# Optimization experiments

Measured on AMD Instinct MI355X. Metric: run time of the kernel, lower is better.

The kernel has to match this reference:

```python
import jax, jax.numpy as jnp
import numpy as np

D = 512
H = 8
HD = D // H
EPS = 1e-8


def setup_inputs() -> dict:
    key = jax.random.key(0)
    ks = jax.random.split(key, 16)
    B, S = 4, 2048
    s = lambda n: 1.0 / np.sqrt(n)
    inp = {
        "gene_emb": jax.random.normal(ks[0], (B, S, D), jnp.float32),
        "expr_emb": jax.random.normal(ks[1], (B, S, D), jnp.float32),
        "M": jax.random.uniform(ks[2], (B, S, S), jnp.float32),
        # weights stored (in, out) so y = x @ W + b
        "W_fused": jax.random.normal(ks[3], (2 * D, D), jnp.float32) * s(2 * D),
        "b_fused": jnp.zeros((D,), jnp.float32),
        "W_Q": jax.random.normal(ks[4], (D, D), jnp.float32) * s(D),
        "b_Q": jnp.zeros((D,), jnp.float32),
        "W_K": jax.random.normal(ks[5], (D, D), jnp.float32) * s(D),
        "b_K": jnp.zeros((D,), jnp.float32),
        "W_V": jax.random.normal(ks[6], (D, D), jnp.float32) * s(D),
        "b_V": jnp.zeros((D,), jnp.float32),
        "W_O": jax.random.normal(ks[7], (D, D), jnp.float32) * s(D),
        "b_O": jnp.zeros((D,), jnp.float32),
    }
    return inp


def reference(gene_emb, expr_emb, M, W_fused, b_fused, W_Q, b_Q, W_K, b_K, W_V, b_V, W_O, b_O):
    B, S, _ = gene_emb.shape
    scale = HD ** (-0.5)
    fused = jnp.concatenate([gene_emb, expr_emb], axis=-1) @ W_fused + b_fused
    # (B,S,D) -> (B,H,S,HD)
    split = lambda x: x.reshape(B, S, H, HD).transpose(0, 2, 1, 3)
    Q = split(fused @ W_Q + b_Q)
    K = split(fused @ W_K + b_K)
    V = split(expr_emb @ W_V + b_V)
    scores = jnp.einsum("bhqd,bhkd->bhqk", Q, K) * scale
    Mg = M[:, None, :, :]  # broadcast over heads
    scores = scores * Mg
    attn = jax.nn.softmax(scores, axis=-1)
    A_sparse = attn * Mg
    norm = jnp.sum(jnp.abs(A_sparse), axis=-1, keepdims=True) + EPS
    A_bar = A_sparse / norm
    out = jnp.einsum("bhqk,bhkd->bhqd", A_bar, V)
    out = out.transpose(0, 2, 1, 3).reshape(B, S, D)
    return out @ W_O + b_O
```

## Files before the change

kernel.cpp:

```cpp
#include <hip/hip_runtime.h>

typedef unsigned short u16;
typedef __attribute__((ext_vector_type(8))) short bf16x8_t;
typedef __attribute__((ext_vector_type(4))) float f32x4_t;

__device__ __forceinline__ u16 f2bf(float x){
  union { float f; unsigned u; } v; v.f = x;
  unsigned r = v.u + 0x7FFFu + ((v.u >> 16) & 1u);
  return (u16)(r >> 16);
}
__device__ __forceinline__ float bf2f(u16 h){
  union { unsigned u; float f; } v; v.u = ((unsigned)h) << 16;
  return v.f;
}
__device__ __forceinline__ u16 hi16(float x){
  union { float f; unsigned u; } v; v.f = x;
  return (u16)(v.u >> 16);
}

__device__ __forceinline__ void gl2lds16(const u16* g, u16* l){
  __builtin_amdgcn_global_load_lds((const __attribute__((address_space(1))) void*)g,
                                   (__attribute__((address_space(3))) void*)l, 16, 0, 0);
}

__global__ __launch_bounds__(256) void prep_kernel(
    const float* __restrict__ gene, const float* __restrict__ expr,
    const float* __restrict__ Wf, const float* __restrict__ Wq,
    const float* __restrict__ Wk, const float* __restrict__ Wv,
    const float* __restrict__ Wo,
    u16* __restrict__ Xh, u16* __restrict__ Xl,
    u16* __restrict__ Wfth, u16* __restrict__ Wftl,
    u16* __restrict__ Wqth, u16* __restrict__ Wkth,
    u16* __restrict__ Wvth, u16* __restrict__ Woth)
{
  __shared__ float t[64][65];
  int tid = threadIdx.x;
  if (blockIdx.x < 8192){
    size_t e = ((size_t)blockIdx.x * 256 + tid) * 4;
    int row = (int)(e >> 10);
    int col = (int)(e & 1023);
    const float* src = (col < 512) ? (gene + (size_t)row * 512 + col)
                                   : (expr + (size_t)row * 512 + (col - 512));
    float4 v = *(const float4*)src;
    float a[4] = {v.x, v.y, v.z, v.w};
    u16 hs[4], ls[4];
#pragma unroll
    for (int i = 0; i < 4; i++){
      hs[i] = f2bf(a[i]);
      ls[i] = f2bf(a[i] - bf2f(hs[i]));
    }
    *(uint2*)(Xh + e) = make_uint2(hs[0] | ((unsigned)hs[1] << 16), hs[2] | ((unsigned)hs[3] << 16));
    *(uint2*)(Xl + e) = make_uint2(ls[0] | ((unsigned)ls[1] << 16), ls[2] | ((unsigned)ls[3] << 16));
    return;
  }
  int id = blockIdx.x - 8192;
  const float* W; u16* Th; u16* Tl; int K, kx, ny;
  if (id < 128){ W = Wf; Th = Wfth; Tl = Wftl; K = 1024; kx = id >> 3; ny = id & 7; }
  else {
    int tt = id - 128; int wi = tt >> 6; tt &= 63; kx = tt >> 3; ny = tt & 7; K = 512;
    W  = (wi == 0) ? Wq  : (wi == 1) ? Wk  : (wi == 2) ? Wv  : Wo;
    Th = (wi == 0) ? Wqth: (wi == 1) ? Wkth: (wi == 2) ? Wvth: Woth;
    Tl = nullptr;
  }
  int k0 = kx * 64, n0 = ny * 64;
  int r = tid >> 4;
  int c4 = (tid & 15) * 4;
#pragma unroll
  for (int p = 0; p < 4; p++){
    int k = p * 16 + r;
    float4 v = *(const float4*)(W + (size_t)(k0 + k) * 512 + n0 + c4);
    t[c4 + 0][k] = v.x; t[c4 + 1][k] = v.y; t[c4 + 2][k] = v.z; t[c4 + 3][k] = v.w;
  }
  __syncthreads();
#pragma unroll
  for (int p = 0; p < 4; p++){
    int n = p * 16 + r;
    u16 hs[4], ls[4];
#pragma unroll
    for (int i = 0; i < 4; i++){
      float x = t[n][c4 + i];
      hs[i] = f2bf(x);
      ls[i] = f2bf(x - bf2f(hs[i]));
    }
    size_t o = (size_t)(n0 + n) * K + k0 + c4;
    *(uint2*)(Th + o) = make_uint2(hs[0] | ((unsigned)hs[1] << 16), hs[2] | ((unsigned)hs[3] << 16));
    if (Tl)
      *(uint2*)(Tl + o) = make_uint2(ls[0] | ((unsigned)ls[1] << 16), ls[2] | ((unsigned)ls[3] << 16));
  }
}

template<int SPLITS>
__device__ __forceinline__ void gemm_core(
    const u16* __restrict__ Ah, const u16* __restrict__ Al, int lda,
    const u16* __restrict__ Bh, const u16* __restrict__ Bl, int K,
    int m0, int n0, f32x4_t (&acc)[4][2],
    u16* sAh, u16* sAl, u16* sBh, u16* sBl)
{
  int tid = threadIdx.x;
  int lane = tid & 63, w = tid >> 6, quad = lane >> 4, l15 = lane & 15;
  int wm = w & 1, wn = w >> 1;
  int lrow = lane >> 2;
  int swzS = ((lane >> 2) & 3) ^ ((lane >> 4) & 3);
  int gkq  = ((lane & 3) ^ swzS) * 8;
  const u16* pA0 = Ah + (size_t)(m0 + w * 32 + lrow) * lda + gkq;
  const u16* pA1 = Ah + (size_t)(m0 + w * 32 + 16 + lrow) * lda + gkq;
  const u16* pL0 = (SPLITS >= 2) ? Al + (size_t)(m0 + w * 32 + lrow) * lda + gkq : nullptr;
  const u16* pL1 = (SPLITS >= 2) ? Al + (size_t)(m0 + w * 32 + 16 + lrow) * lda + gkq : nullptr;
  const u16* pB0 = Bh + (size_t)(n0 + w * 16 + lrow) * K + gkq;
  const u16* pBl = (SPLITS == 3) ? Bl + (size_t)(n0 + w * 16 + lrow) * K + gkq : nullptr;
  u16* dA  = sAh + w * 1024;
  u16* dAl = (SPLITS >= 2) ? sAl + w * 1024 : nullptr;
  u16* dB  = sBh + w * 512;
  u16* dBl = (SPLITS == 3) ? sBl + w * 512 : nullptr;
  int pq = (quad ^ ((l15 & 3) ^ ((l15 >> 2) & 3))) * 8;

  for (int k0 = 0; k0 < K; k0 += 64){
    __syncthreads();
#pragma unroll
    for (int hf = 0; hf < 2; hf++){
      gl2lds16(pA0 + k0 + hf * 32, dA + hf * 4096);
      gl2lds16(pA1 + k0 + hf * 32, dA + hf * 4096 + 512);
      if constexpr (SPLITS >= 2){
        gl2lds16(pL0 + k0 + hf * 32, dAl + hf * 4096);
        gl2lds16(pL1 + k0 + hf * 32, dAl + hf * 4096 + 512);
      }
      gl2lds16(pB0 + k0 + hf * 32, dB + hf * 2048);
      if constexpr (SPLITS == 3)
        gl2lds16(pBl + k0 + hf * 32, dBl + hf * 2048);
    }
    __syncthreads();

#pragma unroll
    for (int hf = 0; hf < 2; hf++){
      bf16x8_t aH[4], aL[4], bH[2], bL[2];
#pragma unroll
      for (int mi = 0; mi < 4; mi++){
        int ad = (wm * 64 + mi * 16 + l15) * 32 + pq + hf * 4096;
        aH[mi] = *(const bf16x8_t*)&sAh[ad];
        if constexpr (SPLITS >= 2) aL[mi] = *(const bf16x8_t*)&sAl[ad];
      }
#pragma unroll
      for (int ni = 0; ni < 2; ni++){
        int bd = (wn * 32 + ni * 16 + l15) * 32 + pq + hf * 2048;
        bH[ni] = *(const bf16x8_t*)&sBh[bd];
        if constexpr (SPLITS == 3) bL[ni] = *(const bf16x8_t*)&sBl[bd];
      }
#pragma unroll
      for (int mi = 0; mi < 4; mi++)
#pragma unroll
        for (int ni = 0; ni < 2; ni++){
          acc[mi][ni] = __builtin_amdgcn_mfma_f32_16x16x32_bf16(aH[mi], bH[ni], acc[mi][ni], 0, 0, 0);
          if constexpr (SPLITS == 3)
            acc[mi][ni] = __builtin_amdgcn_mfma_f32_16x16x32_bf16(aH[mi], bL[ni], acc[mi][ni], 0, 0, 0);
          if constexpr (SPLITS >= 2)
            acc[mi][ni] = __builtin_amdgcn_mfma_f32_16x16x32_bf16(aL[mi], bH[ni], acc[mi][ni], 0, 0, 0);
        }
    }
  }
}

__global__ __launch_bounds__(256, 2) void gemm_fused_kernel(
    const u16* __restrict__ Xh, const u16* __restrict__ Xl,
    const u16* __restrict__ Wfth, const u16* __restrict__ Wftl,
    const float* __restrict__ bias, u16* __restrict__ Fh, u16* __restrict__ Fl)
{
  __shared__ __align__(16) u16 sAh[128 * 64], sAl[128 * 64], sBh[64 * 64], sBl[64 * 64];
  int m0 = blockIdx.x * 128, n0 = blockIdx.y * 64;
  f32x4_t acc[4][2];
#pragma unroll
  for (int i = 0; i < 4; i++)
#pragma unroll
    for (int j = 0; j < 2; j++)
#pragma unroll
      for (int r = 0; r < 4; r++) acc[i][j][r] = 0.f;
  gemm_core<3>(Xh, Xl, 1024, Wfth, Wftl, 1024, m0, n0, acc, sAh, sAl, sBh, sBl);

  int lane = threadIdx.x & 63, w = threadIdx.x >> 6, quad = lane >> 4, l15 = lane & 15;
  int wm = w & 1, wn = w >> 1;
#pragma unroll
  for (int mi = 0; mi < 4; mi++)
#pragma unroll
    for (int ni = 0; ni < 2; ni++){
      int gn = n0 + wn * 32 + ni * 16 + l15;
      float bs = bias[gn];
      int gm0 = m0 + wm * 64 + mi * 16 + quad * 4;
#pragma unroll
      for (int r = 0; r < 4; r++){
        float v = acc[mi][ni][r] + bs;
        u16 hb = f2bf(v);
        Fh[(size_t)(gm0 + r) * 512 + gn] = hb;
        Fl[(size_t)(gm0 + r) * 512 + gn] = f2bf(v - bf2f(hb));
      }
    }
}

__global__ __launch_bounds__(256, 2) void gemm_qkv_kernel(
    const u16* __restrict__ Fh, const u16* __restrict__ Fl,
    const u16* __restrict__ Xeh, const u16* __restrict__ Xel,
    const u16* __restrict__ Wqth, const u16* __restrict__ Wkth, const u16* __restrict__ Wvth,
    const float* __restrict__ bq, const float* __restrict__ bk, const float* __restrict__ bv,
    u16* __restrict__ Q, u16* __restrict__ Kout, u16* __restrict__ Vt, float qsc)
{
  __shared__ __align__(16) u16 sAh[128 * 64], sAl[128 * 64], sBh[64 * 64];
  int side = blockIdx.y >> 3;
  int m0 = blockIdx.x * 128, n0 = (blockIdx.y & 7) * 64;
  const u16* Ah = (side == 2) ? Xeh : Fh;
  const u16* Al = (side == 2) ? Xel : Fl;
  int lda = (side == 2) ? 1024 : 512;
  const u16* Bh = (side == 0) ? Wqth : (side == 1) ? Wkth : Wvth;
  const float* bias = (side == 0) ? bq : (side == 1) ? bk : bv;

  f32x4_t acc[4][2];
#pragma unroll
  for (int i = 0; i < 4; i++)
#pragma unroll
    for (int j = 0; j < 2; j++)
#pragma unroll
      for (int r = 0; r < 4; r++) acc[i][j][r] = 0.f;
  gemm_core<2>(Ah, Al, lda, Bh, nullptr, 512, m0, n0, acc, sAh, sAl, sBh, nullptr);

  int lane = threadIdx.x & 63, w = threadIdx.x >> 6, quad = lane >> 4, l15 = lane & 15;
  int wm = w & 1, wn = w >> 1;
#pragma unroll
  for (int mi = 0; mi < 4; mi++)
#pragma unroll
    for (int ni = 0; ni < 2; ni++){
      int gn = n0 + wn * 32 + ni * 16 + l15;
      float bs = bias[gn];
      int gm0 = m0 + wm * 64 + mi * 16 + quad * 4;
#pragma unroll
      for (int r = 0; r < 4; r++){
        float v = acc[mi][ni][r] + bs;
        int gm = gm0 + r;
        if (side == 0){
          Q[(size_t)gm * 512 + gn] = f2bf(v * qsc);
        } else if (side == 1){
          Kout[(size_t)gm * 512 + gn] = f2bf(v);
        } else {
          int bb = gm >> 11, s = gm & 2047;
          int hh = gn >> 6, d = gn & 63;
          Vt[((size_t)((bb * 8 + hh) * 64 + d) << 11) + s] = f2bf(v);
        }
      }
    }
}

__global__ __launch_bounds__(256, 2) void gemm_o_kernel(
    const u16* __restrict__ Oh, const u16* __restrict__ Woth,
    const float* __restrict__ bias, float* __restrict__ out)
{
  __shared__ __align__(16) u16 sAh[128 * 64], sBh[64 * 64];
  int m0 = blockIdx.x * 128, n0 = blockIdx.y * 64;
  f32x4_t acc[4][2];
#pragma unroll
  for (int i = 0; i < 4; i++)
#pragma unroll
    for (int j = 0; j < 2; j++)
#pragma unroll
      for (int r = 0; r < 4; r++) acc[i][j][r] = 0.f;
  gemm_core<1>(Oh, nullptr, 512, Woth, nullptr, 512, m0, n0, acc, sAh, nullptr, sBh, nullptr);

  int lane = threadIdx.x & 63, w = threadIdx.x >> 6, quad = lane >> 4, l15 = lane & 15;
  int wm = w & 1, wn = w >> 1;
#pragma unroll
  for (int mi = 0; mi < 4; mi++)
#pragma unroll
    for (int ni = 0; ni < 2; ni++){
      int gn = n0 + wn * 32 + ni * 16 + l15;
      float bs = bias[gn];
      int gm0 = m0 + wm * 64 + mi * 16 + quad * 4;
#pragma unroll
      for (int r = 0; r < 4; r++)
        out[(size_t)(gm0 + r) * 512 + gn] = acc[mi][ni][r] + bs;
    }
}

__global__ __launch_bounds__(256, 3) void flash_kernel(
    const u16* __restrict__ Qh, const u16* __restrict__ Kh,
    const u16* __restrict__ Vt, const float* __restrict__ Mm,
    u16* __restrict__ Oh)
{
  __shared__ __align__(16) u16 sKh[2 * 4096], sVt[2 * 4096];
  __shared__ __align__(16) u16 sP[64 * 72];
  int tid = threadIdx.x, lane = tid & 63, w = tid >> 6, quad = lane >> 4, l15 = lane & 15;
  int bh = blockIdx.y, b = bh >> 3, h = bh & 7;
  int q0 = blockIdx.x * 64;

  int qrow = q0 + w * 16 + l15;
  const u16* qp = Qh + ((size_t)(b * 2048 + qrow)) * 512 + h * 64 + quad * 8;
  bf16x8_t qH[2];
  qH[0] = *(const bf16x8_t*)qp;  qH[1] = *(const bf16x8_t*)(qp + 32);

  float lp[4] = {0.f, 0.f, 0.f, 0.f};
  f32x4_t Oacc[4];
#pragma unroll
  for (int ni = 0; ni < 4; ni++)
#pragma unroll
    for (int r = 0; r < 4; r++) Oacc[ni][r] = 0.f;

  int srow = lane >> 3;
  int gc = ((lane & 7) ^ srow) * 8;
  const u16* gKh0 = Kh + ((size_t)(b * 2048 + w * 16 + srow)) * 512 + h * 64 + gc;
  const u16* gVt0 = Vt + ((size_t)(bh * 64 + w * 16 + srow)) * 2048 + gc;
  const float* Mbase = Mm + (size_t)b * 2048 * 2048 + (size_t)(q0 + w * 16) * 2048;

  gl2lds16(gKh0,            sKh + w * 1024);
  gl2lds16(gKh0 + 8 * 512,  sKh + w * 1024 + 512);
  gl2lds16(gVt0,            sVt + w * 1024);
  gl2lds16(gVt0 + 8 * 2048, sVt + w * 1024 + 512);

  float Mc[4][4];
#pragma unroll
  for (int ni = 0; ni < 4; ni++)
#pragma unroll
    for (int r = 0; r < 4; r++)
      Mc[ni][r] = Mbase[(size_t)(quad * 4 + r) * 2048 + ni * 16 + l15];

  int sw7 = l15 & 7;
  for (int it = 0; it < 32; ++it){
    int k0 = it * 64;
    const u16* cK = sKh + (it & 1) * 4096;
    const u16* cV = sVt + (it & 1) * 4096;
    __syncthreads();

    bool hasNext = (it + 1) < 32;
    if (hasNext){
      int kn = k0 + 64;
      u16* nK = sKh + ((it + 1) & 1) * 4096 + w * 1024;
      u16* nV = sVt + ((it + 1) & 1) * 4096 + w * 1024;
      gl2lds16(gKh0 + (size_t)kn * 512,       nK);
      gl2lds16(gKh0 + (size_t)(kn + 8) * 512, nK + 512);
      gl2lds16(gVt0 + kn,                     nV);
      gl2lds16(gVt0 + 8 * 2048 + kn,          nV + 512);
    }

    float Mn[4][4];
    if (hasNext){
#pragma unroll
      for (int ni = 0; ni < 4; ni++)
#pragma unroll
        for (int r = 0; r < 4; r++)
          Mn[ni][r] = Mbase[(size_t)(quad * 4 + r) * 2048 + (k0 + 64) + ni * 16 + l15];
    }

    f32x4_t S[4];
#pragma unroll
    for (int ni = 0; ni < 4; ni++)
#pragma unroll
      for (int r = 0; r < 4; r++) S[ni][r] = 0.f;
#pragma unroll
    for (int ni = 0; ni < 4; ni++){
      int kb = (ni * 16 + l15) * 64;
#pragma unroll
      for (int ds = 0; ds < 2; ds++){
        int p = ((ds * 4 + quad) ^ sw7) * 8;
        bf16x8_t kf = *(const bf16x8_t*)&cK[kb + p];
        S[ni] = __builtin_amdgcn_mfma_f32_16x16x32_bf16(qH[ds], kf, S[ni], 0, 0, 0);
      }
    }

#pragma unroll
    for (int ni = 0; ni < 4; ni++)
#pragma unroll
      for (int r = 0; r < 4; r++){
        float m = Mc[ni][r];
        float p = m * __builtin_amdgcn_exp2f(S[ni][r] * m);
        lp[r] += p;
        sP[(w * 16 + quad * 4 + r) * 72 + ni * 16 + l15] = hi16(p);
      }

#pragma unroll
    for (int ds = 0; ds < 2; ds++){
      bf16x8_t pf = *(const bf16x8_t*)&sP[(w * 16 + l15) * 72 + ds * 32 + quad * 8];
#pragma unroll
      for (int ni = 0; ni < 4; ni++){
        int p = ((ds * 4 + quad) ^ sw7) * 8;
        bf16x8_t vf = *(const bf16x8_t*)&cV[(ni * 16 + l15) * 64 + p];
        Oacc[ni] = __builtin_amdgcn_mfma_f32_16x16x32_bf16(pf, vf, Oacc[ni], 0, 0, 0);
      }
    }

    if (hasNext){
#pragma unroll
      for (int ni = 0; ni < 4; ni++)
#pragma unroll
        for (int r = 0; r < 4; r++) Mc[ni][r] = Mn[ni][r];
    }
  }

#pragma unroll
  for (int r = 0; r < 4; r++){
#pragma unroll
    for (int off = 1; off < 16; off <<= 1)
      lp[r] += __shfl_xor(lp[r], off);
  }

#pragma unroll
  for (int r = 0; r < 4; r++){
    float inv = 1.0f / lp[r];
    int q = q0 + w * 16 + quad * 4 + r;
    size_t rb = ((size_t)(b * 2048 + q)) * 512 + h * 64;
#pragma unroll
    for (int ni = 0; ni < 4; ni++)
      Oh[rb + ni * 16 + l15] = f2bf(Oacc[ni][r] * inv);
  }
}

extern "C" void kernel_launch(void* const* d_in, const int* in_sizes, int n_in,
                              void* d_out, int out_size, void* d_ws, size_t ws_size,
                              hipStream_t stream)
{
  const float* gene = (const float*)d_in[0];
  const float* expr = (const float*)d_in[1];
  const float* Mm   = (const float*)d_in[2];
  const float* Wf   = (const float*)d_in[3];
  const float* bfv  = (const float*)d_in[4];
  const float* Wq   = (const float*)d_in[5];
  const float* bq   = (const float*)d_in[6];
  const float* Wk   = (const float*)d_in[7];
  const float* bk   = (const float*)d_in[8];
  const float* Wv   = (const float*)d_in[9];
  const float* bv   = (const float*)d_in[10];
  const float* Wo   = (const float*)d_in[11];
  const float* bo   = (const float*)d_in[12];
  float* out = (float*)d_out;

  char* ws = (char*)d_ws;
  size_t off = 0;
  auto alloc = [&](size_t bytes) -> void* {
    void* p = (void*)(ws + off);
    off += (bytes + 255) & ~(size_t)255;
    return p;
  };
  u16* Xh   = (u16*)alloc(8192ull * 1024 * 2);
  u16* Xl   = (u16*)alloc(8192ull * 1024 * 2);
  u16* Wfth = (u16*)alloc(512ull * 1024 * 2);
  u16* Wftl = (u16*)alloc(512ull * 1024 * 2);
  u16* Wqth = (u16*)alloc(512ull * 512 * 2);
  u16* Wkth = (u16*)alloc(512ull * 512 * 2);
  u16* Wvth = (u16*)alloc(512ull * 512 * 2);
  u16* Woth = (u16*)alloc(512ull * 512 * 2);
  u16* Fh   = (u16*)alloc(8192ull * 512 * 2);
  u16* Fl   = (u16*)alloc(8192ull * 512 * 2);
  u16* Qh   = (u16*)alloc(8192ull * 512 * 2);
  u16* Kh   = (u16*)alloc(8192ull * 512 * 2);
  u16* Vt   = (u16*)alloc(8192ull * 512 * 2);
  u16* Oh = Xh;

  const float QSC = 0.1803368801f;

  prep_kernel<<<8576, 256, 0, stream>>>(gene, expr, Wf, Wq, Wk, Wv, Wo,
                                        Xh, Xl, Wfth, Wftl, Wqth, Wkth, Wvth, Woth);
  gemm_fused_kernel<<<dim3(64, 8), 256, 0, stream>>>(Xh, Xl, Wfth, Wftl, bfv, Fh, Fl);
  gemm_qkv_kernel<<<dim3(64, 24), 256, 0, stream>>>(Fh, Fl, Xh + 512, Xl + 512,
                                                    Wqth, Wkth, Wvth, bq, bk, bv,
                                                    Qh, Kh, Vt, QSC);
  flash_kernel<<<dim3(32, 32), 256, 0, stream>>>(Qh, Kh, Vt, Mm, Oh);
  gemm_o_kernel<<<dim3(64, 8), 256, 0, stream>>>(Oh, Woth, bo, out);

  (void)in_sizes; (void)n_in; (void)out_size; (void)ws_size;
}
```

Baseline: 339.5 us.

## Fold fused projection into Q/K weights, double-buffer GEMMs, swizzle flash P tile

Precomputes W_fused·W_Q and W_fused·W_K (plus folded biases) inside the prep kernel, so Q and K come straight from the concatenated input in a single GEMM and the separate fused GEMM and its F intermediate disappear. The GEMM core gains LDS double buffering and drops the 3-way split precision on the weight side. The flash kernel gets an XOR-swizzled P buffer instead of a padded one and higher occupancy via launch bounds. These cut a kernel launch and a large intermediate round trip, in exchange for a small fp32 weight-product GEMM in prep and some precision loss from rounding the folded weights to bf16.

```diff
diff --git a/kernel.cpp b/kernel.cpp
--- a/kernel.cpp
+++ b/kernel.cpp
@@ -28,12 +28,12 @@
     const float* __restrict__ Wf, const float* __restrict__ Wq,
     const float* __restrict__ Wk, const float* __restrict__ Wv,
     const float* __restrict__ Wo,
+    const float* __restrict__ bfv, const float* __restrict__ bq, const float* __restrict__ bk,
     u16* __restrict__ Xh, u16* __restrict__ Xl,
-    u16* __restrict__ Wfth, u16* __restrict__ Wftl,
-    u16* __restrict__ Wqth, u16* __restrict__ Wkth,
-    u16* __restrict__ Wvth, u16* __restrict__ Woth)
-{
-  __shared__ float t[64][65];
+    u16* __restrict__ Wfqt, u16* __restrict__ Wfkt,
+    u16* __restrict__ Wvth, u16* __restrict__ Woth,
+    float* __restrict__ bfq, float* __restrict__ bfk)
+{
   int tid = threadIdx.x;
   if (blockIdx.x < 8192){
     size_t e = ((size_t)blockIdx.x * 256 + tid) * 4;
@@ -54,48 +54,101 @@
     return;
   }
   int id = blockIdx.x - 8192;
-  const float* W; u16* Th; u16* Tl; int K, kx, ny;
-  if (id < 128){ W = Wf; Th = Wfth; Tl = Wftl; K = 1024; kx = id >> 3; ny = id & 7; }
-  else {
-    int tt = id - 128; int wi = tt >> 6; tt &= 63; kx = tt >> 3; ny = tt & 7; K = 512;
-    W  = (wi == 0) ? Wq  : (wi == 1) ? Wk  : (wi == 2) ? Wv  : Wo;
-    Th = (wi == 0) ? Wqth: (wi == 1) ? Wkth: (wi == 2) ? Wvth: Woth;
-    Tl = nullptr;
-  }
+  if (id < 128){
+    __shared__ float t[64][65];
+    const float* W = (id < 64) ? Wv : Wo;
+    u16* Th = (id < 64) ? Wvth : Woth;
+    int tt = id & 63;
+    int k0 = (tt >> 3) * 64, n0 = (tt & 7) * 64;
+    int r = tid >> 4;
+    int c4 = (tid & 15) * 4;
+#pragma unroll
+    for (int p = 0; p < 4; p++){
+      int k = p * 16 + r;
+      float4 v = *(const float4*)(W + (size_t)(k0 + k) * 512 + n0 + c4);
+      t[c4 + 0][k] = v.x; t[c4 + 1][k] = v.y; t[c4 + 2][k] = v.z; t[c4 + 3][k] = v.w;
+    }
+    __syncthreads();
+#pragma unroll
+    for (int p = 0; p < 4; p++){
+      int n = p * 16 + r;
+      u16 hs[4];
+#pragma unroll
+      for (int i = 0; i < 4; i++) hs[i] = f2bf(t[n][c4 + i]);
+      size_t o = (size_t)(n0 + n) * 512 + k0 + c4;
+      *(uint2*)(Th + o) = make_uint2(hs[0] | ((unsigned)hs[1] << 16), hs[2] | ((unsigned)hs[3] << 16));
+    }
+    return;
+  }
+  id -= 128;
+  int mat = id >> 7;
+  int t2 = id & 127;
+  int kx = t2 >> 3, ny = t2 & 7;
+  const float* Wsec = mat ? Wk : Wq;
+  u16* Outp = mat ? Wfkt : Wfqt;
+  float* bout = mat ? bfk : bfq;
+  const float* bsec = mat ? bk : bq;
   int k0 = kx * 64, n0 = ny * 64;
-  int r = tid >> 4;
-  int c4 = (tid & 15) * 4;
-#pragma unroll
-  for (int p = 0; p < 4; p++){
-    int k = p * 16 + r;
-    float4 v = *(const float4*)(W + (size_t)(k0 + k) * 512 + n0 + c4);
-    t[c4 + 0][k] = v.x; t[c4 + 1][k] = v.y; t[c4 + 2][k] = v.z; t[c4 + 3][k] = v.w;
-  }
-  __syncthreads();
-#pragma unroll
-  for (int p = 0; p < 4; p++){
-    int n = p * 16 + r;
-    u16 hs[4], ls[4];
-#pragma unroll
-    for (int i = 0; i < 4; i++){
-      float x = t[n][c4 + i];
-      hs[i] = f2bf(x);
-      ls[i] = f2bf(x - bf2f(hs[i]));
-    }
-    size_t o = (size_t)(n0 + n) * K + k0 + c4;
-    *(uint2*)(Th + o) = make_uint2(hs[0] | ((unsigned)hs[1] << 16), hs[2] | ((unsigned)hs[3] << 16));
-    if (Tl)
-      *(uint2*)(Tl + o) = make_uint2(ls[0] | ((unsigned)ls[1] << 16), ls[2] | ((unsigned)ls[3] << 16));
-  }
-}
-
-template<int SPLITS>
-__device__ __forceinline__ void gemm_core(
+  __shared__ float sF[32][65];
+  __shared__ float sQm[32][65];
+  float acc[4][4];
+#pragma unroll
+  for (int i = 0; i < 4; i++)
+#pragma unroll
+    for (int j = 0; j < 4; j++) acc[i][j] = 0.f;
+  int tn = tid & 15, tk = tid >> 4;
+  for (int jc = 0; jc < 512; jc += 32){
+    __syncthreads();
+    {
+      int k = tid >> 2;
+      int j0 = (tid & 3) * 8;
+      float4 v0 = *(const float4*)(Wf + (size_t)(k0 + k) * 512 + jc + j0);
+      float4 v1 = *(const float4*)(Wf + (size_t)(k0 + k) * 512 + jc + j0 + 4);
+      sF[j0 + 0][k] = v0.x; sF[j0 + 1][k] = v0.y; sF[j0 + 2][k] = v0.z; sF[j0 + 3][k] = v0.w;
+      sF[j0 + 4][k] = v1.x; sF[j0 + 5][k] = v1.y; sF[j0 + 6][k] = v1.z; sF[j0 + 7][k] = v1.w;
+    }
+    {
+      int j = tid >> 3;
+      int n8 = (tid & 7) * 8;
+      float4 v0 = *(const float4*)(Wsec + (size_t)(jc + j) * 512 + n0 + n8);
+      float4 v1 = *(const float4*)(Wsec + (size_t)(jc + j) * 512 + n0 + n8 + 4);
+      sQm[j][n8 + 0] = v0.x; sQm[j][n8 + 1] = v0.y; sQm[j][n8 + 2] = v0.z; sQm[j][n8 + 3] = v0.w;
+      sQm[j][n8 + 4] = v1.x; sQm[j][n8 + 5] = v1.y; sQm[j][n8 + 6] = v1.z; sQm[j][n8 + 7] = v1.w;
+    }
+    __syncthreads();
+#pragma unroll 8
+    for (int j = 0; j < 32; j++){
+      float a[4], bb[4];
+#pragma unroll
+      for (int i = 0; i < 4; i++){ a[i] = sQm[j][tn * 4 + i]; bb[i] = sF[j][tk * 4 + i]; }
+#pragma unroll
+      for (int kk = 0; kk < 4; kk++)
+#pragma unroll
+        for (int nn = 0; nn < 4; nn++) acc[kk][nn] += bb[kk] * a[nn];
+    }
+  }
+#pragma unroll
+  for (int nn = 0; nn < 4; nn++)
+#pragma unroll
+    for (int kk = 0; kk < 4; kk++)
+      Outp[(size_t)(n0 + tn * 4 + nn) * 1024 + k0 + tk * 4 + kk] = f2bf(acc[kk][nn]);
+  if (kx == 0 && tid < 64){
+    float s = 0.f;
+    for (int j = 0; j < 512; j++) s += bfv[j] * Wsec[(size_t)j * 512 + n0 + tid];
+    bout[n0 + tid] = s + bsec[n0 + tid];
+  }
+}
+
+template<int SPLITS, int BK>
+__device__ __forceinline__ void gemm_core_db(
     const u16* __restrict__ Ah, const u16* __restrict__ Al, int lda,
-    const u16* __restrict__ Bh, const u16* __restrict__ Bl, int K,
+    const u16* __restrict__ Bh, int K,
     int m0, int n0, f32x4_t (&acc)[4][2],
-    u16* sAh, u16* sAl, u16* sBh, u16* sBl)
-{
+    u16* sAh, u16* sAl, u16* sBh)
+{
+  constexpr int NH  = BK / 32;
+  constexpr int ASZ = 128 * BK;
+  constexpr int BSZ = 64 * BK;
   int tid = threadIdx.x;
   int lane = tid & 63, w = tid >> 6, quad = lane >> 4, l15 = lane & 15;
   int wm = w & 1, wn = w >> 1;
@@ -107,51 +160,50 @@
   const u16* pL0 = (SPLITS >= 2) ? Al + (size_t)(m0 + w * 32 + lrow) * lda + gkq : nullptr;
   const u16* pL1 = (SPLITS >= 2) ? Al + (size_t)(m0 + w * 32 + 16 + lrow) * lda + gkq : nullptr;
   const u16* pB0 = Bh + (size_t)(n0 + w * 16 + lrow) * K + gkq;
-  const u16* pBl = (SPLITS == 3) ? Bl + (size_t)(n0 + w * 16 + lrow) * K + gkq : nullptr;
-  u16* dA  = sAh + w * 1024;
-  u16* dAl = (SPLITS >= 2) ? sAl + w * 1024 : nullptr;
-  u16* dB  = sBh + w * 512;
-  u16* dBl = (SPLITS == 3) ? sBl + w * 512 : nullptr;
   int pq = (quad ^ ((l15 & 3) ^ ((l15 >> 2) & 3))) * 8;
-
-  for (int k0 = 0; k0 < K; k0 += 64){
-    __syncthreads();
-#pragma unroll
-    for (int hf = 0; hf < 2; hf++){
+  const int NIT = K / BK;
+
+  auto stage = [&](int it){
+    int bi = it & 1, k0 = it * BK;
+    u16* dA = sAh + bi * ASZ + w * 1024;
+    u16* dB = sBh + bi * BSZ + w * 512;
+#pragma unroll
+    for (int hf = 0; hf < NH; hf++){
       gl2lds16(pA0 + k0 + hf * 32, dA + hf * 4096);
       gl2lds16(pA1 + k0 + hf * 32, dA + hf * 4096 + 512);
       if constexpr (SPLITS >= 2){
+        u16* dAl = sAl + bi * ASZ + w * 1024;
         gl2lds16(pL0 + k0 + hf * 32, dAl + hf * 4096);
         gl2lds16(pL1 + k0 + hf * 32, dAl + hf * 4096 + 512);
       }
       gl2lds16(pB0 + k0 + hf * 32, dB + hf * 2048);
-      if constexpr (SPLITS == 3)
-        gl2lds16(pBl + k0 + hf * 32, dBl + hf * 2048);
-    }
+    }
+  };
+
+  stage(0);
+  for (int it = 0; it < NIT; ++it){
+    int bi = it & 1;
     __syncthreads();
-
-#pragma unroll
-    for (int hf = 0; hf < 2; hf++){
-      bf16x8_t aH[4], aL[4], bH[2], bL[2];
+    if (it + 1 < NIT) stage(it + 1);
+#pragma unroll
+    for (int hf = 0; hf < NH; hf++){
+      bf16x8_t aH[4], aL[4], bH[2];
 #pragma unroll
       for (int mi = 0; mi < 4; mi++){
-        int ad = (wm * 64 + mi * 16 + l15) * 32 + pq + hf * 4096;
+        int ad = (wm * 64 + mi * 16 + l15) * 32 + pq + bi * ASZ + hf * 4096;
         aH[mi] = *(const bf16x8_t*)&sAh[ad];
         if constexpr (SPLITS >= 2) aL[mi] = *(const bf16x8_t*)&sAl[ad];
       }
 #pragma unroll
       for (int ni = 0; ni < 2; ni++){
-        int bd = (wn * 32 + ni * 16 + l15) * 32 + pq + hf * 2048;
+        int bd = (wn * 32 + ni * 16 + l15) * 32 + pq + bi * BSZ + hf * 2048;
         bH[ni] = *(const bf16x8_t*)&sBh[bd];
-        if constexpr (SPLITS == 3) bL[ni] = *(const bf16x8_t*)&sBl[bd];
       }
 #pragma unroll
       for (int mi = 0; mi < 4; mi++)
 #pragma unroll
         for (int ni = 0; ni < 2; ni++){
           acc[mi][ni] = __builtin_amdgcn_mfma_f32_16x16x32_bf16(aH[mi], bH[ni], acc[mi][ni], 0, 0, 0);
-          if constexpr (SPLITS == 3)
-            acc[mi][ni] = __builtin_amdgcn_mfma_f32_16x16x32_bf16(aH[mi], bL[ni], acc[mi][ni], 0, 0, 0);
           if constexpr (SPLITS >= 2)
             acc[mi][ni] = __builtin_amdgcn_mfma_f32_16x16x32_bf16(aL[mi], bH[ni], acc[mi][ni], 0, 0, 0);
         }
@@ -159,56 +211,23 @@
   }
 }
 
-__global__ __launch_bounds__(256, 2) void gemm_fused_kernel(
+__global__ __launch_bounds__(256, 3) void gemm_qkv_kernel(
     const u16* __restrict__ Xh, const u16* __restrict__ Xl,
-    const u16* __restrict__ Wfth, const u16* __restrict__ Wftl,
-    const float* __restrict__ bias, u16* __restrict__ Fh, u16* __restrict__ Fl)
-{
-  __shared__ __align__(16) u16 sAh[128 * 64], sAl[128 * 64], sBh[64 * 64], sBl[64 * 64];
-  int m0 = blockIdx.x * 128, n0 = blockIdx.y * 64;
-  f32x4_t acc[4][2];
-#pragma unroll
-  for (int i = 0; i < 4; i++)
-#pragma unroll
-    for (int j = 0; j < 2; j++)
-#pragma unroll
-      for (int r = 0; r < 4; r++) acc[i][j][r] = 0.f;
-  gemm_core<3>(Xh, Xl, 1024, Wfth, Wftl, 1024, m0, n0, acc, sAh, sAl, sBh, sBl);
-
-  int lane = threadIdx.x & 63, w = threadIdx.x >> 6, quad = lane >> 4, l15 = lane & 15;
-  int wm = w & 1, wn = w >> 1;
-#pragma unroll
-  for (int mi = 0; mi < 4; mi++)
-#pragma unroll
-    for (int ni = 0; ni < 2; ni++){
-      int gn = n0 + wn * 32 + ni * 16 + l15;
-      float bs = bias[gn];
-      int gm0 = m0 + wm * 64 + mi * 16 + quad * 4;
-#pragma unroll
-      for (int r = 0; r < 4; r++){
-        float v = acc[mi][ni][r] + bs;
-        u16 hb = f2bf(v);
-        Fh[(size_t)(gm0 + r) * 512 + gn] = hb;
-        Fl[(size_t)(gm0 + r) * 512 + gn] = f2bf(v - bf2f(hb));
-      }
-    }
-}
-
-__global__ __launch_bounds__(256, 2) void gemm_qkv_kernel(
-    const u16* __restrict__ Fh, const u16* __restrict__ Fl,
-    const u16* __restrict__ Xeh, const u16* __restrict__ Xel,
-    const u16* __restrict__ Wqth, const u16* __restrict__ Wkth, const u16* __restrict__ Wvth,
-    const float* __restrict__ bq, const float* __restrict__ bk, const float* __restrict__ bv,
+    const u16* __restrict__ Wfqt, const u16* __restrict__ Wfkt, const u16* __restrict__ Wvth,
+    const float* __restrict__ bfq, const float* __restrict__ bfk, const float* __restrict__ bv,
     u16* __restrict__ Q, u16* __restrict__ Kout, u16* __restrict__ Vt, float qsc)
 {
-  __shared__ __align__(16) u16 sAh[128 * 64], sAl[128 * 64], sBh[64 * 64];
+  __shared__ __align__(16) u16 sAh[2 * 4096], sAl[2 * 4096], sBh[2 * 2048];
+  __shared__ u16 sPad[6144];
+  if (qsc < 0.f){ sPad[threadIdx.x] = 0; __syncthreads(); sAh[0] = sPad[0]; }
+
   int side = blockIdx.y >> 3;
   int m0 = blockIdx.x * 128, n0 = (blockIdx.y & 7) * 64;
-  const u16* Ah = (side == 2) ? Xeh : Fh;
-  const u16* Al = (side == 2) ? Xel : Fl;
-  int lda = (side == 2) ? 1024 : 512;
-  const u16* Bh = (side == 0) ? Wqth : (side == 1) ? Wkth : Wvth;
-  const float* bias = (side == 0) ? bq : (side == 1) ? bk : bv;
+  const u16* Ah = (side == 2) ? Xh + 512 : Xh;
+  const u16* Al = (side == 2) ? Xl + 512 : Xl;
+  int K = (side == 2) ? 512 : 1024;
+  const u16* Bh = (side == 0) ? Wfqt : (side == 1) ? Wfkt : Wvth;
+  const float* bias = (side == 0) ? bfq : (side == 1) ? bfk : bv;
 
   f32x4_t acc[4][2];
 #pragma unroll
@@ -217,7 +236,7 @@
     for (int j = 0; j < 2; j++)
 #pragma unroll
       for (int r = 0; r < 4; r++) acc[i][j][r] = 0.f;
-  gemm_core<2>(Ah, Al, lda, Bh, nullptr, 512, m0, n0, acc, sAh, sAl, sBh, nullptr);
+  gemm_core_db<2, 32>(Ah, Al, 1024, Bh, K, m0, n0, acc, sAh, sAl, sBh);
 
   int lane = threadIdx.x & 63, w = threadIdx.x >> 6, quad = lane >> 4, l15 = lane & 15;
   int wm = w & 1, wn = w >> 1;
@@ -249,7 +268,7 @@
     const u16* __restrict__ Oh, const u16* __restrict__ Woth,
     const float* __restrict__ bias, float* __restrict__ out)
 {
-  __shared__ __align__(16) u16 sAh[128 * 64], sBh[64 * 64];
+  __shared__ __align__(16) u16 sAh[2 * 8192], sBh[2 * 4096];
   int m0 = blockIdx.x * 128, n0 = blockIdx.y * 64;
   f32x4_t acc[4][2];
 #pragma unroll
@@ -258,7 +277,7 @@
     for (int j = 0; j < 2; j++)
 #pragma unroll
       for (int r = 0; r < 4; r++) acc[i][j][r] = 0.f;
-  gemm_core<1>(Oh, nullptr, 512, Woth, nullptr, 512, m0, n0, acc, sAh, nullptr, sBh, nullptr);
+  gemm_core_db<1, 64>(Oh, nullptr, 512, Woth, 512, m0, n0, acc, sAh, nullptr, sBh);
 
   int lane = threadIdx.x & 63, w = threadIdx.x >> 6, quad = lane >> 4, l15 = lane & 15;
   int wm = w & 1, wn = w >> 1;
@@ -275,13 +294,12 @@
     }
 }
 
-__global__ __launch_bounds__(256, 3) void flash_kernel(
+__global__ __launch_bounds__(256, 4) void flash_kernel(
     const u16* __restrict__ Qh, const u16* __restrict__ Kh,
     const u16* __restrict__ Vt, const float* __restrict__ Mm,
     u16* __restrict__ Oh)
 {
-  __shared__ __align__(16) u16 sKh[2 * 4096], sVt[2 * 4096];
-  __shared__ __align__(16) u16 sP[64 * 72];
+  __shared__ __align__(16) u16 sKh[2 * 4096], sVt[2 * 4096], sP[4096];
   int tid = threadIdx.x, lane = tid & 63, w = tid >> 6, quad = lane >> 4, l15 = lane & 15;
   int bh = blockIdx.y, b = bh >> 3, h = bh & 7;
   int q0 = blockIdx.x * 64;
@@ -300,14 +318,21 @@
 
   int srow = lane >> 3;
   int gc = ((lane & 7) ^ srow) * 8;
-  const u16* gKh0 = Kh + ((size_t)(b * 2048 + w * 16 + srow)) * 512 + h * 64 + gc;
-  const u16* gVt0 = Vt + ((size_t)(bh * 64 + w * 16 + srow)) * 2048 + gc;
+  const u16* gK = Kh + ((size_t)(b * 2048 + w * 16 + srow)) * 512 + h * 64 + gc;
+  const u16* gV = Vt + ((size_t)(bh * 64 + w * 16 + srow)) * 2048 + gc;
+
+  auto stage = [&](int it){
+    int bi = it & 1, k0 = it * 64;
+    u16* dK = sKh + bi * 4096 + w * 1024;
+    u16* dV = sVt + bi * 4096 + w * 1024;
+    gl2lds16(gK + (size_t)k0 * 512,       dK);
+    gl2lds16(gK + (size_t)(k0 + 8) * 512, dK + 512);
+    gl2lds16(gV + k0,                     dV);
+    gl2lds16(gV + 8 * 2048 + k0,          dV + 512);
+  };
+
   const float* Mbase = Mm + (size_t)b * 2048 * 2048 + (size_t)(q0 + w * 16) * 2048;
-
-  gl2lds16(gKh0,            sKh + w * 1024);
-  gl2lds16(gKh0 + 8 * 512,  sKh + w * 1024 + 512);
-  gl2lds16(gVt0,            sVt + w * 1024);
-  gl2lds16(gVt0 + 8 * 2048, sVt + w * 1024 + 512);
+  stage(0);
 
   float Mc[4][4];
 #pragma unroll
@@ -318,29 +343,21 @@
 
   int sw7 = l15 & 7;
   for (int it = 0; it < 32; ++it){
-    int k0 = it * 64;
-    const u16* cK = sKh + (it & 1) * 4096;
-    const u16* cV = sVt + (it & 1) * 4096;
+    int bi = it & 1;
+    const u16* cK = sKh + bi * 4096;
+    const u16* cV = sVt + bi * 4096;
     __syncthreads();
-
     bool hasNext = (it + 1) < 32;
-    if (hasNext){
-      int kn = k0 + 64;
-      u16* nK = sKh + ((it + 1) & 1) * 4096 + w * 1024;
-      u16* nV = sVt + ((it + 1) & 1) * 4096 + w * 1024;
-      gl2lds16(gKh0 + (size_t)kn * 512,       nK);
-      gl2lds16(gKh0 + (size_t)(kn + 8) * 512, nK + 512);
-      gl2lds16(gVt0 + kn,                     nV);
-      gl2lds16(gVt0 + 8 * 2048 + kn,          nV + 512);
-    }
+    if (hasNext) stage(it + 1);
 
     float Mn[4][4];
     if (hasNext){
+      int kn = (it + 1) * 64;
 #pragma unroll
       for (int ni = 0; ni < 4; ni++)
 #pragma unroll
         for (int r = 0; r < 4; r++)
-          Mn[ni][r] = Mbase[(size_t)(quad * 4 + r) * 2048 + (k0 + 64) + ni * 16 + l15];
+          Mn[ni][r] = Mbase[(size_t)(quad * 4 + r) * 2048 + kn + ni * 16 + l15];
     }
 
     f32x4_t S[4];
@@ -353,8 +370,7 @@
       int kb = (ni * 16 + l15) * 64;
 #pragma unroll
       for (int ds = 0; ds < 2; ds++){
-        int p = ((ds * 4 + quad) ^ sw7) * 8;
-        bf16x8_t kf = *(const bf16x8_t*)&cK[kb + p];
+        bf16x8_t kf = *(const bf16x8_t*)&cK[kb + (((ds * 4 + quad) ^ sw7)) * 8];
         S[ni] = __builtin_amdgcn_mfma_f32_16x16x32_bf16(qH[ds], kf, S[ni], 0, 0, 0);
       }
     }
@@ -366,16 +382,17 @@
         float m = Mc[ni][r];
         float p = m * __builtin_amdgcn_exp2f(S[ni][r] * m);
         lp[r] += p;
-        sP[(w * 16 + quad * 4 + r) * 72 + ni * 16 + l15] = hi16(p);
+        int row = quad * 4 + r;
+        int colg = ni * 2 + (l15 >> 3);
+        sP[w * 1024 + row * 64 + ((colg ^ (row & 7)) << 3) + (l15 & 7)] = hi16(p);
       }
 
 #pragma unroll
     for (int ds = 0; ds < 2; ds++){
-      bf16x8_t pf = *(const bf16x8_t*)&sP[(w * 16 + l15) * 72 + ds * 32 + quad * 8];
+      bf16x8_t pf = *(const bf16x8_t*)&sP[w * 1024 + l15 * 64 + (((ds * 4 + quad) ^ sw7) << 3)];
 #pragma unroll
       for (int ni = 0; ni < 4; ni++){
-        int p = ((ds * 4 + quad) ^ sw7) * 8;
-        bf16x8_t vf = *(const bf16x8_t*)&cV[(ni * 16 + l15) * 64 + p];
+        bf16x8_t vf = *(const bf16x8_t*)&cV[(ni * 16 + l15) * 64 + (((ds * 4 + quad) ^ sw7)) * 8];
         Oacc[ni] = __builtin_amdgcn_mfma_f32_16x16x32_bf16(pf, vf, Oacc[ni], 0, 0, 0);
       }
     }
@@ -432,29 +449,25 @@
     off += (bytes + 255) & ~(size_t)255;
     return p;
   };
-  u16* Xh   = (u16*)alloc(8192ull * 1024 * 2);
-  u16* Xl   = (u16*)alloc(8192ull * 1024 * 2);
-  u16* Wfth = (u16*)alloc(512ull * 1024 * 2);
-  u16* Wftl = (u16*)alloc(512ull * 1024 * 2);
-  u16* Wqth = (u16*)alloc(512ull * 512 * 2);
-  u16* Wkth = (u16*)alloc(512ull * 512 * 2);
-  u16* Wvth = (u16*)alloc(512ull * 512 * 2);
-  u16* Woth = (u16*)alloc(512ull * 512 * 2);
-  u16* Fh   = (u16*)alloc(8192ull * 512 * 2);
-  u16* Fl   = (u16*)alloc(8192ull * 512 * 2);
-  u16* Qh   = (u16*)alloc(8192ull * 512 * 2);
-  u16* Kh   = (u16*)alloc(8192ull * 512 * 2);
-  u16* Vt   = (u16*)alloc(8192ull * 512 * 2);
+  u16* Xh    = (u16*)alloc(8192ull * 1024 * 2);
+  u16* Xl    = (u16*)alloc(8192ull * 1024 * 2);
+  u16* Wfqt  = (u16*)alloc(512ull * 1024 * 2);
+  u16* Wfkt  = (u16*)alloc(512ull * 1024 * 2);
+  u16* Wvth  = (u16*)alloc(512ull * 512 * 2);
+  u16* Woth  = (u16*)alloc(512ull * 512 * 2);
+  float* bfq = (float*)alloc(512 * 4);
+  float* bfk = (float*)alloc(512 * 4);
+  u16* Qh    = (u16*)alloc(8192ull * 512 * 2);
+  u16* Kh    = (u16*)alloc(8192ull * 512 * 2);
+  u16* Vt    = (u16*)alloc(8192ull * 512 * 2);
   u16* Oh = Xh;
 
   const float QSC = 0.1803368801f;
 
-  prep_kernel<<<8576, 256, 0, stream>>>(gene, expr, Wf, Wq, Wk, Wv, Wo,
-                                        Xh, Xl, Wfth, Wftl, Wqth, Wkth, Wvth, Woth);
-  gemm_fused_kernel<<<dim3(64, 8), 256, 0, stream>>>(Xh, Xl, Wfth, Wftl, bfv, Fh, Fl);
-  gemm_qkv_kernel<<<dim3(64, 24), 256, 0, stream>>>(Fh, Fl, Xh + 512, Xl + 512,
-                                                    Wqth, Wkth, Wvth, bq, bk, bv,
-                                                    Qh, Kh, Vt, QSC);
+  prep_kernel<<<8576, 256, 0, stream>>>(gene, expr, Wf, Wq, Wk, Wv, Wo, bfv, bq, bk,
+                                        Xh, Xl, Wfqt, Wfkt, Wvth, Woth, bfq, bfk);
+  gemm_qkv_kernel<<<dim3(64, 24), 256, 0, stream>>>(Xh, Xl, Wfqt, Wfkt, Wvth,
+                                                    bfq, bfk, bv, Qh, Kh, Vt, QSC);
   flash_kernel<<<dim3(32, 32), 256, 0, stream>>>(Qh, Kh, Vt, Mm, Oh);
   gemm_o_kernel<<<dim3(64, 8), 256, 0, stream>>>(Oh, Woth, bo, out);
 
```

Result: slower. 377.7 us (+11.3%).
